# Kernel optimization log

Measured on AMD Instinct MI355X. Metric: run time of the kernel, lower is better.

The kernel has to match this reference:

```python
import jax, jax.numpy as jnp
import numpy as np

E, C, F, K = 8, 768, 3072, 2  # NUM_EXPERTS, EMBED_DIM, FFN_DIM, TOP_K


def setup_inputs() -> dict:
    key = jax.random.key(0)
    k0, k1, k2, k3 = jax.random.split(key, 4)
    B, T = 8, 2048
    return {
        "x": jax.random.normal(k0, (B, T, C), jnp.float32),
        "router_w": jax.random.normal(k1, (E, C), jnp.float32) * 0.02,
        "w1": jax.random.normal(k2, (E, C, F), jnp.float32) * 0.02,
        "b1": jnp.zeros((E, F), jnp.float32),
        "w2": jax.random.normal(k3, (E, F, C), jnp.float32) * 0.02,
        "b2": jnp.zeros((E, C), jnp.float32),
    }


def reference(x, router_w, w1, b1, w2, b2):
    # Dropout is inference-mode identity (eval). GELU is torch's exact (erf) variant.
    B, T, Cc = x.shape
    flat = x.reshape(-1, Cc)                                   # [N, C]
    logits = flat @ router_w.T                                 # [N, E]
    probs = jax.nn.softmax(logits.astype(jnp.float32), axis=-1)
    top_w, top_i = jax.lax.top_k(probs, K)                     # [N, K]
    top_w = (top_w / top_w.sum(-1, keepdims=True)).astype(x.dtype)
    out = jnp.zeros_like(flat)
    for e in range(E):
        # per-token combine weight for expert e (0 if token not routed to e)
        w_e = jnp.sum(top_w * (top_i == e), axis=-1)[:, None]  # [N, 1]
        h = jax.nn.gelu(flat @ w1[e] + b1[e], approximate=False)  # [N, F]
        out = out + w_e * (h @ w2[e] + b2[e])
    return out.reshape(B, T, Cc)
```

## Files before the change

### kernel.cpp

```cpp
#include <hip/hip_runtime.h>
#include <hip/hip_bf16.h>

#define NTOK 16384
#define CDIM 768
#define FDIM 3072
#define NEXP 8
#define NSLOT 32768
#define HBLK 128
#define MAXTILES 263

typedef __attribute__((ext_vector_type(8))) short bf16x8;
typedef __attribute__((ext_vector_type(4))) float f32x4;
typedef __attribute__((ext_vector_type(8))) unsigned short u16x8;

__device__ __forceinline__ unsigned short f2bf(float f) {
  unsigned int u = __float_as_uint(f);
  u += 0x7FFFu + ((u >> 16) & 1u);
  return (unsigned short)(u >> 16);
}
__device__ __forceinline__ float bf2f(unsigned short h) {
  return __uint_as_float((unsigned int)h << 16);
}

__device__ __forceinline__ void async16(const void* g, void* l) {
  __builtin_amdgcn_global_load_lds(
      (const __attribute__((address_space(1))) unsigned int*)g,
      (__attribute__((address_space(3))) unsigned int*)l, 16, 0, 0);
}

__global__ __launch_bounds__(256)
void k_transpose(const float* __restrict__ src, unsigned short* __restrict__ dst,
                 int R, int Cc)
{
  __shared__ float tle[32][33];
  int e = blockIdx.z;
  int c0 = blockIdx.x * 32, r0 = blockIdx.y * 32;
  int tx = threadIdx.x & 31, ty = threadIdx.x >> 5;
  const float* s = src + (size_t)e * R * Cc;
  unsigned short* d = dst + (size_t)e * R * Cc;
#pragma unroll
  for (int i = 0; i < 4; ++i)
    tle[ty + i * 8][tx] = s[(size_t)(r0 + ty + i * 8) * Cc + c0 + tx];
  __syncthreads();
#pragma unroll
  for (int i = 0; i < 4; ++i)
    d[(size_t)(c0 + ty + i * 8) * R + r0 + tx] = f2bf(tle[tx][ty + i * 8]);
}

__global__ __launch_bounds__(256)
void k_router(const float* __restrict__ x, const float* __restrict__ rw,
              int* __restrict__ tk_e, float* __restrict__ tk_w)
{
  __shared__ float srw[NEXP * CDIM];
  int tid = threadIdx.x;
#pragma unroll
  for (int i = 0; i < (NEXP * CDIM / 4) / 256; ++i)
    ((float4*)srw)[tid + i * 256] = ((const float4*)rw)[tid + i * 256];
  __syncthreads();
  int lane = tid & 63, wid = tid >> 6;
  int t = blockIdx.x * 4 + wid;
  float a[NEXP];
#pragma unroll
  for (int e = 0; e < NEXP; ++e) a[e] = 0.f;
  const float* xr = x + (size_t)t * CDIM;
#pragma unroll
  for (int c = 0; c < CDIM / 64; ++c) {
    float xv = xr[c * 64 + lane];
#pragma unroll
    for (int e = 0; e < NEXP; ++e) a[e] += xv * srw[e * CDIM + c * 64 + lane];
  }
#pragma unroll
  for (int e = 0; e < NEXP; ++e) {
#pragma unroll
    for (int off = 32; off; off >>= 1) a[e] += __shfl_xor(a[e], off);
  }
  if (lane == 0) {
    int i0 = 0; float l0 = a[0];
#pragma unroll
    for (int e = 1; e < NEXP; ++e) if (a[e] > l0) { l0 = a[e]; i0 = e; }
    int i1 = -1; float l1 = -1e30f;
#pragma unroll
    for (int e = 0; e < NEXP; ++e) if (e != i0 && a[e] > l1) { l1 = a[e]; i1 = e; }
    float w0 = 1.f / (1.f + expf(l1 - l0));
    tk_e[2 * t] = i0;     tk_e[2 * t + 1] = i1;
    tk_w[2 * t] = w0;     tk_w[2 * t + 1] = 1.f - w0;
  }
}

__global__ __launch_bounds__(256)
void k_hist(const int* __restrict__ tk_e, int* __restrict__ blockhist)
{
  __shared__ int h[NEXP];
  int tid = threadIdx.x;
  if (tid < NEXP) h[tid] = 0;
  __syncthreads();
  int e = tk_e[blockIdx.x * 256 + tid];
  atomicAdd(&h[e], 1);
  __syncthreads();
  if (tid < NEXP) blockhist[blockIdx.x * NEXP + tid] = h[tid];
}

__global__ __launch_bounds__(512)
void k_scan2(const int* __restrict__ blockhist, int* __restrict__ counts,
             int* __restrict__ offsets, int* __restrict__ tp,
             int* __restrict__ blockbase)
{
  __shared__ int ltot[NEXP];
  __shared__ int loff[NEXP + 1];
  int tid = threadIdx.x;
  int lane = tid & 63, e = tid >> 6;
  int o0 = blockhist[lane * NEXP + e];
  int o1 = blockhist[(64 + lane) * NEXP + e];
  int h0 = o0, h1 = o1;
#pragma unroll
  for (int d = 1; d < 64; d <<= 1) { int v = __shfl_up(h0, d); if (lane >= d) h0 += v; }
  int s0 = __shfl(h0, 63);
#pragma unroll
  for (int d = 1; d < 64; d <<= 1) { int v = __shfl_up(h1, d); if (lane >= d) h1 += v; }
  h1 += s0;
  if (lane == 63) ltot[e] = h1;
  __syncthreads();
  if (tid == 0) {
    loff[0] = 0;
    int tpv = 0; tp[0] = 0;
    for (int k = 0; k < NEXP; ++k) {
      loff[k + 1] = loff[k] + ltot[k];
      counts[k] = ltot[k];
      offsets[k] = loff[k];
      tpv += (ltot[k] + 127) / 128;
      tp[k + 1] = tpv;
    }
    offsets[NEXP] = loff[NEXP];
  }
  __syncthreads();
  int base = loff[e];
  blockbase[lane * NEXP + e]        = base + h0 - o0;
  blockbase[(64 + lane) * NEXP + e] = base + h1 - o1;
}

__global__ __launch_bounds__(256)
void k_assign_gather(const float* __restrict__ x, const int* __restrict__ tk_e,
                     const float* __restrict__ tk_w,
                     const int* __restrict__ blockbase,
                     int* __restrict__ tok2slot, float* __restrict__ slot_w,
                     unsigned short* __restrict__ Xg)
{
  __shared__ int eh[256];
  __shared__ int sslot[256];
  int b = blockIdx.x, tid = threadIdx.x;
  int pick = b * 256 + tid;
  int e = tk_e[pick];
  eh[tid] = e;
  __syncthreads();
  int rank = 0;
  for (int j = 0; j < tid; ++j) rank += (eh[j] == e);
  int slot = blockbase[b * NEXP + e] + rank;
  sslot[tid] = slot;
  tok2slot[pick] = slot;
  slot_w[slot] = tk_w[pick];
  __syncthreads();
  int lane = tid & 63, wid = tid >> 6;
  for (int p = wid * 64; p < wid * 64 + 64; ++p) {
    int token = (b * 256 + p) >> 1;
    int s = sslot[p];
    const float4* src = (const float4*)(x + (size_t)token * CDIM);
    ushort4* dst = (ushort4*)(Xg + (size_t)s * CDIM);
#pragma unroll
    for (int i = 0; i < 3; ++i) {
      float4 v = src[i * 64 + lane];
      ushort4 hh;
      hh.x = f2bf(v.x); hh.y = f2bf(v.y); hh.z = f2bf(v.z); hh.w = f2bf(v.w);
      dst[i * 64 + lane] = hh;
    }
  }
}

template <int EPI>
__device__ __forceinline__ void gemm_body(
    const unsigned short* __restrict__ A, int lda,
    const unsigned short* __restrict__ B, int ldb, long sB,
    int Ksteps,
    const int* __restrict__ counts, const int* __restrict__ offsets,
    const int* __restrict__ tp, int t0,
    const float* __restrict__ bias, int biasStride,
    unsigned short* __restrict__ Hout, int ldh,
    unsigned short* __restrict__ Yout, const float* __restrict__ slot_w,
    int gx, int nwg)
{
  __shared__ __align__(16) char lds[3 * 16384];

  int orig = blockIdx.y * gx + blockIdx.x;
  int q = nwg >> 3, r = nwg & 7;
  int xcd = orig & 7, jj = orig >> 3;
  int wgid = (xcd < r ? xcd * (q + 1) : r * (q + 1) + (xcd - r) * q) + jj;
  const int RG = 16;
  int yT = nwg / gx;
  int gsize = gx * RG;
  int rg = wgid / gsize;
  int rem = wgid - rg * gsize;
  int rgs = yT - rg * RG; if (rgs > RG) rgs = RG;
  int bx = rem / rgs;
  int byl = rg * RG + (rem - bx * rgs);
  int by = t0 + byl;

  if (by >= tp[NEXP]) return;
  int e = 0;
  while (by >= tp[e + 1]) ++e;
  int m0 = (by - tp[e]) * 128;
  int cnt = counts[e];
  int rowbase = offsets[e];
  int n0 = bx * 128;

  const unsigned short* Bexp = B + (long)e * sB + (long)n0 * ldb;
  const unsigned short* Aexp =
      (EPI == 0) ? A + (long)(rowbase + m0) * lda
                 : A + (long)(byl * 128) * lda;

  int tid = threadIdx.x;
  int lane = tid & 63, wid = tid >> 6;
  int wm = wid >> 1, wn = wid & 1;
  int ar = lane & 15, kg = lane >> 4;
  int kgs = (kg ^ ((ar >> 1) & 3)) << 4;

  int rA0 = tid >> 2;
  int cA0 = tid & 3;
  int ksw = (cA0 ^ ((rA0 >> 1) & 3)) << 3;
  const unsigned short* As0 = Aexp + (long)rA0 * lda + ksw;
  const unsigned short* As1 = Aexp + (long)(rA0 + 64) * lda + ksw;
  const unsigned short* Bs0 = Bexp + (long)rA0 * ldb + ksw;
  const unsigned short* Bs1 = Bexp + (long)(rA0 + 64) * ldb + ksw;

  f32x4 acc[4][4] = {};

  auto STAGE = [&](int buf, int t) {
    char* bb = lds + buf * 16384;
    int ko = t * 32;
    async16(As0 + ko, bb + wid * 1024);
    async16(As1 + ko, bb + 4096 + wid * 1024);
    async16(Bs0 + ko, bb + 8192 + wid * 1024);
    async16(Bs1 + ko, bb + 12288 + wid * 1024);
  };

  STAGE(0, 0); STAGE(1, 1);
  int cur = 0;
  int nxt2 = 2;

  for (int ks = 0; ks < Ksteps; ++ks) {
    if (ks + 2 < Ksteps) {
      asm volatile("s_waitcnt vmcnt(4)" ::: "memory");
    } else if (ks + 1 < Ksteps) {
      asm volatile("s_waitcnt vmcnt(4)" ::: "memory");
    } else {
      asm volatile("s_waitcnt vmcnt(0)" ::: "memory");
    }
    __builtin_amdgcn_s_barrier();
    asm volatile("" ::: "memory");

    const char* bb = lds + cur * 16384;
    const char* bA = bb + (wm * 64 + ar) * 64 + kgs;
    const char* bB = bb + 8192 + (wn * 64 + ar) * 64 + kgs;
    bf16x8 af[4], bfr[4];
#pragma unroll
    for (int i = 0; i < 4; ++i) af[i] = *(const bf16x8*)(bA + i * 1024);
#pragma unroll
    for (int i = 0; i < 4; ++i) bfr[i] = *(const bf16x8*)(bB + i * 1024);

    if (ks + 2 < Ksteps) STAGE(nxt2, ks + 2);

#pragma unroll
    for (int mi = 0; mi < 4; ++mi)
#pragma unroll
      for (int ni = 0; ni < 4; ++ni)
        acc[mi][ni] = __builtin_amdgcn_mfma_f32_16x16x32_bf16(af[mi], bfr[ni],
                                                              acc[mi][ni], 0, 0, 0);
    cur = (cur == 2) ? 0 : cur + 1;
    nxt2 = (nxt2 == 2) ? 0 : nxt2 + 1;
  }

  unsigned short* st = (unsigned short*)lds;
  __syncthreads();

  if (EPI == 0) {
#pragma unroll
    for (int ni = 0; ni < 4; ++ni) {
      int col = wn * 64 + ni * 16 + ar;
      float bv = bias[e * biasStride + n0 + col];
#pragma unroll
      for (int mi = 0; mi < 4; ++mi) {
#pragma unroll
        for (int rr = 0; rr < 4; ++rr) {
          int row = wm * 64 + mi * 16 + kg * 4 + rr;
          float v = acc[mi][ni][rr] + bv;
          v = 0.5f * v * (1.0f + erff(v * 0.70710678118654752f));
          st[row * 136 + col] = f2bf(v);
        }
      }
    }
    __syncthreads();
    int row = tid >> 1, half = tid & 1;
    unsigned short* drow = Hout + (long)(byl * 128 + row) * ldh + n0 + half * 64;
    const unsigned short* srow = st + row * 136 + half * 64;
#pragma unroll
    for (int i = 0; i < 8; ++i)
      *(u16x8*)(drow + i * 8) = *(const u16x8*)(srow + i * 8);
  } else {
#pragma unroll
    for (int mi = 0; mi < 4; ++mi) {
#pragma unroll
      for (int rr = 0; rr < 4; ++rr) {
        int rowl = wm * 64 + mi * 16 + kg * 4 + rr;
        float wt = (m0 + rowl < cnt) ? slot_w[rowbase + m0 + rowl] : 0.f;
#pragma unroll
        for (int ni = 0; ni < 4; ++ni) {
          int col = wn * 64 + ni * 16 + ar;
          float v = (acc[mi][ni][rr] + bias[e * biasStride + n0 + col]) * wt;
          st[rowl * 136 + col] = f2bf(v);
        }
      }
    }
    __syncthreads();
    int row = tid >> 1, half = tid & 1;
    if (m0 + row < cnt) {
      unsigned short* drow = Yout + (long)(rowbase + m0 + row) * CDIM + n0 + half * 64;
      const unsigned short* srow = st + row * 136 + half * 64;
#pragma unroll
      for (int i = 0; i < 8; ++i)
        *(u16x8*)(drow + i * 8) = *(const u16x8*)(srow + i * 8);
    }
  }
}

__global__ __launch_bounds__(256, 3)
void k_gemm1(const unsigned short* __restrict__ A, int lda,
             const unsigned short* __restrict__ B, int ldb, long sB,
             int Ksteps, const int* __restrict__ counts,
             const int* __restrict__ offsets, const int* __restrict__ tp,
             int t0, const float* __restrict__ bias, int biasStride,
             unsigned short* __restrict__ Hout, int ldh, int gx, int nwg)
{
  gemm_body<0>(A, lda, B, ldb, sB, Ksteps, counts, offsets, tp, t0,
               bias, biasStride, Hout, ldh, nullptr, nullptr, gx, nwg);
}

__global__ __launch_bounds__(256, 3)
void k_gemm2(const unsigned short* __restrict__ A, int lda,
             const unsigned short* __restrict__ B, int ldb, long sB,
             int Ksteps, const int* __restrict__ counts,
             const int* __restrict__ offsets, const int* __restrict__ tp,
             int t0, const float* __restrict__ bias, int biasStride,
             unsigned short* __restrict__ Yout, const float* __restrict__ slot_w,
             int gx, int nwg)
{
  gemm_body<1>(A, lda, B, ldb, sB, Ksteps, counts, offsets, tp, t0,
               bias, biasStride, nullptr, 0, Yout, slot_w, gx, nwg);
}

__global__ __launch_bounds__(256)
void k_combine(const unsigned short* __restrict__ Y,
               const int* __restrict__ tok2slot, float* __restrict__ out)
{
  int t = blockIdx.x * 4 + (threadIdx.x >> 6);
  int lane = threadIdx.x & 63;
  int s0 = tok2slot[2 * t], s1 = tok2slot[2 * t + 1];
  const ushort4* y0 = (const ushort4*)(Y + (size_t)s0 * CDIM);
  const ushort4* y1 = (const ushort4*)(Y + (size_t)s1 * CDIM);
  float4* o = (float4*)(out + (size_t)t * CDIM);
#pragma unroll
  for (int i = 0; i < 3; ++i) {
    ushort4 a = y0[i * 64 + lane];
    ushort4 b = y1[i * 64 + lane];
    float4 r;
    r.x = bf2f(a.x) + bf2f(b.x);
    r.y = bf2f(a.y) + bf2f(b.y);
    r.z = bf2f(a.z) + bf2f(b.z);
    r.w = bf2f(a.w) + bf2f(b.w);
    o[i * 64 + lane] = r;
  }
}

extern "C" void kernel_launch(void* const* d_in, const int* in_sizes, int n_in,
                              void* d_out, int out_size, void* d_ws, size_t ws_size,
                              hipStream_t stream) {
  const float* x        = (const float*)d_in[0];
  const float* router_w = (const float*)d_in[1];
  const float* w1       = (const float*)d_in[2];
  const float* b1       = (const float*)d_in[3];
  const float* w2       = (const float*)d_in[4];
  const float* b2       = (const float*)d_in[5];
  float* out = (float*)d_out;

  char* ws = (char*)d_ws;
  size_t off = 0;
  auto alloc = [&](size_t bytes) -> void* {
    void* p = ws + off;
    off = (off + bytes + 255) & ~(size_t)255;
    return p;
  };
  int*   counts     = (int*)alloc(NEXP * 4);
  int*   offsets    = (int*)alloc((NEXP + 1) * 4);
  int*   tp         = (int*)alloc((NEXP + 1) * 4);
  int*   tk_e       = (int*)alloc((size_t)NSLOT * 4);
  float* tk_w       = (float*)alloc((size_t)NSLOT * 4);
  int*   blockhist  = (int*)alloc((size_t)HBLK * NEXP * 4);
  int*   blockbase  = (int*)alloc((size_t)HBLK * NEXP * 4);
  int*   tok2slot   = (int*)alloc((size_t)NSLOT * 4);
  float* slot_w     = (float*)alloc((size_t)NSLOT * 4);
  unsigned short* Yslot = (unsigned short*)alloc((size_t)NSLOT * CDIM * 2);
  unsigned short* w1t = (unsigned short*)alloc((size_t)NEXP * FDIM * CDIM * 2);
  unsigned short* w2t = (unsigned short*)alloc((size_t)NEXP * CDIM * FDIM * 2);
  unsigned short* Xg  = (unsigned short*)alloc((size_t)(NSLOT + 128) * CDIM * 2);
  int TPC = 66;
  if (off + ((size_t)TPC * 128 + 128) * FDIM * 2 > ws_size) TPC = 33;
  unsigned short* H = (unsigned short*)alloc(((size_t)TPC * 128 + 128) * FDIM * 2);

  k_transpose<<<dim3(FDIM / 32, CDIM / 32, NEXP), 256, 0, stream>>>(w1, w1t, CDIM, FDIM);
  k_transpose<<<dim3(CDIM / 32, FDIM / 32, NEXP), 256, 0, stream>>>(w2, w2t, FDIM, CDIM);
  k_router<<<NTOK / 4, 256, 0, stream>>>(x, router_w, tk_e, tk_w);
  k_hist<<<HBLK, 256, 0, stream>>>(tk_e, blockhist);
  k_scan2<<<1, 512, 0, stream>>>(blockhist, counts, offsets, tp, blockbase);
  k_assign_gather<<<HBLK, 256, 0, stream>>>(x, tk_e, tk_w, blockbase,
                                            tok2slot, slot_w, Xg);

  for (int t0 = 0; t0 < MAXTILES; t0 += TPC) {
    int yT = (MAXTILES - t0 < TPC) ? (MAXTILES - t0) : TPC;
    int gx1 = FDIM / 128;
    k_gemm1<<<dim3(gx1, yT), 256, 0, stream>>>(
        Xg, CDIM, w1t, CDIM, (long)FDIM * CDIM, CDIM / 32,
        counts, offsets, tp, t0, b1, FDIM, H, FDIM, gx1, gx1 * yT);
    int gx2 = CDIM / 128;
    k_gemm2<<<dim3(gx2, yT), 256, 0, stream>>>(
        H, FDIM, w2t, FDIM, (long)CDIM * FDIM, FDIM / 32,
        counts, offsets, tp, t0, b2, CDIM, Yslot, slot_w, gx2, gx2 * yT);
  }
  k_combine<<<NTOK / 4, 256, 0, stream>>>(Yslot, tok2slot, out);
}
```

Baseline: 682.5 us.

## Widen first expert GEMM tile to 128x256 with 512-thread workgroups

Splits the shared GEMM template into two kernels and gives the up-projection GEMM a 128x256 output tile computed by eight waves, with a three-stage LDS buffer of 24 KB per stage. The point is to halve how often the gathered activation tile is re-read per output column and to cut the number of workgroups. Also simplifies the wait-count logic and enlarges the Xg padding. The trade-off is higher LDS use per workgroup and a tight register budget under launch_bounds(512,4), which could cause spills or lower occupancy.

```diff
diff --git a/kernel.cpp b/kernel.cpp
--- a/kernel.cpp
+++ b/kernel.cpp
@@ -175,19 +175,15 @@
   }
 }
 
-template <int EPI>
-__device__ __forceinline__ void gemm_body(
-    const unsigned short* __restrict__ A, int lda,
-    const unsigned short* __restrict__ B, int ldb, long sB,
-    int Ksteps,
-    const int* __restrict__ counts, const int* __restrict__ offsets,
-    const int* __restrict__ tp, int t0,
-    const float* __restrict__ bias, int biasStride,
-    unsigned short* __restrict__ Hout, int ldh,
-    unsigned short* __restrict__ Yout, const float* __restrict__ slot_w,
-    int gx, int nwg)
-{
-  __shared__ __align__(16) char lds[3 * 16384];
+__global__ __launch_bounds__(512, 4)
+void k_gemm1(const unsigned short* __restrict__ A, int lda,
+             const unsigned short* __restrict__ B, int ldb, long sB,
+             int Ksteps, const int* __restrict__ counts,
+             const int* __restrict__ offsets, const int* __restrict__ tp,
+             int t0, const float* __restrict__ bias, int biasStride,
+             unsigned short* __restrict__ Hout, int ldh, int gx, int nwg)
+{
+  __shared__ __align__(16) char lds[3 * 24576];
 
   int orig = blockIdx.y * gx + blockIdx.x;
   int q = nwg >> 3, r = nwg & 7;
@@ -209,12 +205,129 @@
   int m0 = (by - tp[e]) * 128;
   int cnt = counts[e];
   int rowbase = offsets[e];
+  int n0 = bx * 256;
+
+  const unsigned short* Bexp = B + (long)e * sB + (long)n0 * ldb;
+  const unsigned short* Aexp = A + (long)(rowbase + m0) * lda;
+
+  int tid = threadIdx.x;
+  int lane = tid & 63, wid = tid >> 6;
+  int wm = wid >> 2, wn = wid & 3;
+  int ar = lane & 15, kg = lane >> 4;
+  int kgs = (kg ^ ((ar >> 1) & 3)) << 4;
+
+  int rA0 = tid >> 2;
+  int cA0 = tid & 3;
+  int ksw = (cA0 ^ ((rA0 >> 1) & 3)) << 3;
+  const unsigned short* As0 = Aexp + (long)rA0 * lda + ksw;
+  const unsigned short* Bs0 = Bexp + (long)rA0 * ldb + ksw;
+  const unsigned short* Bs1 = Bexp + (long)(rA0 + 128) * ldb + ksw;
+
+  f32x4 acc[4][4] = {};
+
+  auto STAGE = [&](int buf, int t) {
+    char* bb = lds + buf * 24576;
+    int ko = t * 32;
+    async16(As0 + ko, bb + wid * 1024);
+    async16(Bs0 + ko, bb + 8192 + wid * 1024);
+    async16(Bs1 + ko, bb + 16384 + wid * 1024);
+  };
+
+  STAGE(0, 0); STAGE(1, 1);
+  int cur = 0, nxt2 = 2;
+
+  for (int ks = 0; ks < Ksteps; ++ks) {
+    if (ks + 1 < Ksteps) {
+      asm volatile("s_waitcnt vmcnt(3)" ::: "memory");
+    } else {
+      asm volatile("s_waitcnt vmcnt(0)" ::: "memory");
+    }
+    __builtin_amdgcn_s_barrier();
+    asm volatile("" ::: "memory");
+
+    const char* bb = lds + cur * 24576;
+    const char* bA = bb + (wm * 64 + ar) * 64 + kgs;
+    const char* bB = bb + 8192 + (wn * 64 + ar) * 64 + kgs;
+    bf16x8 af[4], bfr[4];
+#pragma unroll
+    for (int i = 0; i < 4; ++i) af[i] = *(const bf16x8*)(bA + i * 1024);
+#pragma unroll
+    for (int i = 0; i < 4; ++i) bfr[i] = *(const bf16x8*)(bB + i * 1024);
+
+    if (ks + 2 < Ksteps) STAGE(nxt2, ks + 2);
+
+#pragma unroll
+    for (int mi = 0; mi < 4; ++mi)
+#pragma unroll
+      for (int ni = 0; ni < 4; ++ni)
+        acc[mi][ni] = __builtin_amdgcn_mfma_f32_16x16x32_bf16(af[mi], bfr[ni],
+                                                              acc[mi][ni], 0, 0, 0);
+    cur = (cur == 2) ? 0 : cur + 1;
+    nxt2 = (nxt2 == 2) ? 0 : nxt2 + 1;
+  }
+
+  unsigned short* st = (unsigned short*)lds;
+  __syncthreads();
+
+#pragma unroll
+  for (int ni = 0; ni < 4; ++ni) {
+    int col = wn * 64 + ni * 16 + ar;
+    float bv = bias[e * biasStride + n0 + col];
+#pragma unroll
+    for (int mi = 0; mi < 4; ++mi) {
+#pragma unroll
+      for (int rr = 0; rr < 4; ++rr) {
+        int row = wm * 64 + mi * 16 + kg * 4 + rr;
+        float v = acc[mi][ni][rr] + bv;
+        v = 0.5f * v * (1.0f + erff(v * 0.70710678118654752f));
+        st[row * 264 + col] = f2bf(v);
+      }
+    }
+  }
+  __syncthreads();
+  int row = tid >> 2, qq = tid & 3;
+  unsigned short* drow = Hout + (long)(byl * 128 + row) * ldh + n0 + qq * 64;
+  const unsigned short* srow = st + row * 264 + qq * 64;
+#pragma unroll
+  for (int i = 0; i < 8; ++i)
+    *(u16x8*)(drow + i * 8) = *(const u16x8*)(srow + i * 8);
+}
+
+__global__ __launch_bounds__(256, 3)
+void k_gemm2(const unsigned short* __restrict__ A, int lda,
+             const unsigned short* __restrict__ B, int ldb, long sB,
+             int Ksteps, const int* __restrict__ counts,
+             const int* __restrict__ offsets, const int* __restrict__ tp,
+             int t0, const float* __restrict__ bias, int biasStride,
+             unsigned short* __restrict__ Yout, const float* __restrict__ slot_w,
+             int gx, int nwg)
+{
+  __shared__ __align__(16) char lds[3 * 16384];
+
+  int orig = blockIdx.y * gx + blockIdx.x;
+  int q = nwg >> 3, r = nwg & 7;
+  int xcd = orig & 7, jj = orig >> 3;
+  int wgid = (xcd < r ? xcd * (q + 1) : r * (q + 1) + (xcd - r) * q) + jj;
+  const int RG = 16;
+  int yT = nwg / gx;
+  int gsize = gx * RG;
+  int rg = wgid / gsize;
+  int rem = wgid - rg * gsize;
+  int rgs = yT - rg * RG; if (rgs > RG) rgs = RG;
+  int bx = rem / rgs;
+  int byl = rg * RG + (rem - bx * rgs);
+  int by = t0 + byl;
+
+  if (by >= tp[NEXP]) return;
+  int e = 0;
+  while (by >= tp[e + 1]) ++e;
+  int m0 = (by - tp[e]) * 128;
+  int cnt = counts[e];
+  int rowbase = offsets[e];
   int n0 = bx * 128;
 
   const unsigned short* Bexp = B + (long)e * sB + (long)n0 * ldb;
-  const unsigned short* Aexp =
-      (EPI == 0) ? A + (long)(rowbase + m0) * lda
-                 : A + (long)(byl * 128) * lda;
+  const unsigned short* Aexp = A + (long)(byl * 128) * lda;
 
   int tid = threadIdx.x;
   int lane = tid & 63, wid = tid >> 6;
@@ -242,13 +355,10 @@
   };
 
   STAGE(0, 0); STAGE(1, 1);
-  int cur = 0;
-  int nxt2 = 2;
+  int cur = 0, nxt2 = 2;
 
   for (int ks = 0; ks < Ksteps; ++ks) {
-    if (ks + 2 < Ksteps) {
-      asm volatile("s_waitcnt vmcnt(4)" ::: "memory");
-    } else if (ks + 1 < Ksteps) {
+    if (ks + 1 < Ksteps) {
       asm volatile("s_waitcnt vmcnt(4)" ::: "memory");
     } else {
       asm volatile("s_waitcnt vmcnt(0)" ::: "memory");
@@ -280,79 +390,29 @@
   unsigned short* st = (unsigned short*)lds;
   __syncthreads();
 
-  if (EPI == 0) {
-#pragma unroll
-    for (int ni = 0; ni < 4; ++ni) {
-      int col = wn * 64 + ni * 16 + ar;
-      float bv = bias[e * biasStride + n0 + col];
-#pragma unroll
-      for (int mi = 0; mi < 4; ++mi) {
-#pragma unroll
-        for (int rr = 0; rr < 4; ++rr) {
-          int row = wm * 64 + mi * 16 + kg * 4 + rr;
-          float v = acc[mi][ni][rr] + bv;
-          v = 0.5f * v * (1.0f + erff(v * 0.70710678118654752f));
-          st[row * 136 + col] = f2bf(v);
-        }
+#pragma unroll
+  for (int mi = 0; mi < 4; ++mi) {
+#pragma unroll
+    for (int rr = 0; rr < 4; ++rr) {
+      int rowl = wm * 64 + mi * 16 + kg * 4 + rr;
+      float wt = (m0 + rowl < cnt) ? slot_w[rowbase + m0 + rowl] : 0.f;
+#pragma unroll
+      for (int ni = 0; ni < 4; ++ni) {
+        int col = wn * 64 + ni * 16 + ar;
+        float v = (acc[mi][ni][rr] + bias[e * biasStride + n0 + col]) * wt;
+        st[rowl * 136 + col] = f2bf(v);
       }
     }
-    __syncthreads();
-    int row = tid >> 1, half = tid & 1;
-    unsigned short* drow = Hout + (long)(byl * 128 + row) * ldh + n0 + half * 64;
+  }
+  __syncthreads();
+  int row = tid >> 1, half = tid & 1;
+  if (m0 + row < cnt) {
+    unsigned short* drow = Yout + (long)(rowbase + m0 + row) * CDIM + n0 + half * 64;
     const unsigned short* srow = st + row * 136 + half * 64;
 #pragma unroll
     for (int i = 0; i < 8; ++i)
       *(u16x8*)(drow + i * 8) = *(const u16x8*)(srow + i * 8);
-  } else {
-#pragma unroll
-    for (int mi = 0; mi < 4; ++mi) {
-#pragma unroll
-      for (int rr = 0; rr < 4; ++rr) {
-        int rowl = wm * 64 + mi * 16 + kg * 4 + rr;
-        float wt = (m0 + rowl < cnt) ? slot_w[rowbase + m0 + rowl] : 0.f;
-#pragma unroll
-        for (int ni = 0; ni < 4; ++ni) {
-          int col = wn * 64 + ni * 16 + ar;
-          float v = (acc[mi][ni][rr] + bias[e * biasStride + n0 + col]) * wt;
-          st[rowl * 136 + col] = f2bf(v);
-        }
-      }
-    }
-    __syncthreads();
-    int row = tid >> 1, half = tid & 1;
-    if (m0 + row < cnt) {
-      unsigned short* drow = Yout + (long)(rowbase + m0 + row) * CDIM + n0 + half * 64;
-      const unsigned short* srow = st + row * 136 + half * 64;
-#pragma unroll
-      for (int i = 0; i < 8; ++i)
-        *(u16x8*)(drow + i * 8) = *(const u16x8*)(srow + i * 8);
-    }
-  }
-}
-
-__global__ __launch_bounds__(256, 3)
-void k_gemm1(const unsigned short* __restrict__ A, int lda,
-             const unsigned short* __restrict__ B, int ldb, long sB,
-             int Ksteps, const int* __restrict__ counts,
-             const int* __restrict__ offsets, const int* __restrict__ tp,
-             int t0, const float* __restrict__ bias, int biasStride,
-             unsigned short* __restrict__ Hout, int ldh, int gx, int nwg)
-{
-  gemm_body<0>(A, lda, B, ldb, sB, Ksteps, counts, offsets, tp, t0,
-               bias, biasStride, Hout, ldh, nullptr, nullptr, gx, nwg);
-}
-
-__global__ __launch_bounds__(256, 3)
-void k_gemm2(const unsigned short* __restrict__ A, int lda,
-             const unsigned short* __restrict__ B, int ldb, long sB,
-             int Ksteps, const int* __restrict__ counts,
-             const int* __restrict__ offsets, const int* __restrict__ tp,
-             int t0, const float* __restrict__ bias, int biasStride,
-             unsigned short* __restrict__ Yout, const float* __restrict__ slot_w,
-             int gx, int nwg)
-{
-  gemm_body<1>(A, lda, B, ldb, sB, Ksteps, counts, offsets, tp, t0,
-               bias, biasStride, nullptr, 0, Yout, slot_w, gx, nwg);
+  }
 }
 
 __global__ __launch_bounds__(256)
@@ -408,7 +468,7 @@
   unsigned short* Yslot = (unsigned short*)alloc((size_t)NSLOT * CDIM * 2);
   unsigned short* w1t = (unsigned short*)alloc((size_t)NEXP * FDIM * CDIM * 2);
   unsigned short* w2t = (unsigned short*)alloc((size_t)NEXP * CDIM * FDIM * 2);
-  unsigned short* Xg  = (unsigned short*)alloc((size_t)(NSLOT + 128) * CDIM * 2);
+  unsigned short* Xg  = (unsigned short*)alloc((size_t)(NSLOT + 256) * CDIM * 2);
   int TPC = 66;
   if (off + ((size_t)TPC * 128 + 128) * FDIM * 2 > ws_size) TPC = 33;
   unsigned short* H = (unsigned short*)alloc(((size_t)TPC * 128 + 128) * FDIM * 2);
@@ -423,8 +483,8 @@
 
   for (int t0 = 0; t0 < MAXTILES; t0 += TPC) {
     int yT = (MAXTILES - t0 < TPC) ? (MAXTILES - t0) : TPC;
-    int gx1 = FDIM / 128;
-    k_gemm1<<<dim3(gx1, yT), 256, 0, stream>>>(
+    int gx1 = FDIM / 256;
+    k_gemm1<<<dim3(gx1, yT), 512, 0, stream>>>(
         Xg, CDIM, w1t, CDIM, (long)FDIM * CDIM, CDIM / 32,
         counts, offsets, tp, t0, b1, FDIM, H, FDIM, gx1, gx1 * yT);
     int gx2 = CDIM / 128;
```

Result: slower. 699.9 us (+2.5%).
